# Kernel optimization log

Hardware: AMD Instinct MI355X
Metric: run time of the kernel (lower is better)

The kernel has to match this reference:

```python
import jax, jax.numpy as jnp
import numpy as np

B, L, D = 2048, 64, 300   # batch, words per sentence, embedding dim (== kernel_size)
C = 512                    # conv out_channels
H, O = 2048, 1             # fc hidden, fc output


def setup_inputs() -> dict:
    key = jax.random.key(0)
    ks = jax.random.split(key, 8)
    s = 0.05
    return {
        "x1": jax.random.normal(ks[0], (B, L, D), jnp.float32),
        "x2": jax.random.normal(ks[1], (B, L, D), jnp.float32),
        # Conv1d(in=1, out=C, kernel=D) weight is [C,1,D]; stored as [C,D]
        "Wc": jax.random.normal(ks[2], (C, D), jnp.float32) * s,
        "bc": jax.random.normal(ks[3], (C,), jnp.float32) * s,
        "W1": jax.random.normal(ks[4], (H, 2 * C), jnp.float32) * s,
        "b1": jax.random.normal(ks[5], (H,), jnp.float32) * s,
        "W2": jax.random.normal(ks[6], (O, H), jnp.float32) * s,
        "b2": jax.random.normal(ks[7], (O,), jnp.float32) * s,
    }


def reference(x1, x2, Wc, bc, W1, b1, W2, b2):
    # Per-word Conv1d(kernel=D) + ReLU is a full-width filter == linear map D->C.
    # Batch all words in one einsum instead of the original Python loop.
    def encode(x):
        h = jax.nn.relu(jnp.einsum('bld,cd->blc', x, Wc) + bc)  # [B,L,C]
        return jnp.max(h, axis=1)                                # max over words -> [B,C]

    e1 = encode(x1)
    e2 = encode(x2)
    feat = jnp.concatenate([e1 - e2, e1 * e2], axis=1)           # [B,2C]
    h = jnp.tanh(feat @ W1.T + b1)                               # [B,H]
    return h @ W2.T + b2                                         # [B,O]
```

## Files before the change

### kernel.cpp

```cpp
#include <hip/hip_runtime.h>


#define B_SZ 2048
#define L_SZ 64
#define D_SZ 300
#define C_SZ 512
#define H_SZ 2048
#define NKC 40
#define TILE_BYTES 76800
#define BUFSTRIDE 76928

typedef __bf16 bf16x8 __attribute__((ext_vector_type(8)));
typedef float f32x4 __attribute__((ext_vector_type(4)));

__device__ __forceinline__ unsigned short f2bf(float f) {
  unsigned int u = __float_as_uint(f);
  u += 0x7fffu + ((u >> 16) & 1u);
  return (unsigned short)(u >> 16);
}

__device__ __forceinline__ bf16x8 cvt8(float4 v0, float4 v1) {
  bf16x8 r;
  r[0] = (__bf16)v0.x; r[1] = (__bf16)v0.y; r[2] = (__bf16)v0.z; r[3] = (__bf16)v0.w;
  r[4] = (__bf16)v1.x; r[5] = (__bf16)v1.y; r[6] = (__bf16)v1.z; r[7] = (__bf16)v1.w;
  return r;
}

__device__ __forceinline__ void gload_lds16(const float* g, void* l) {
  __builtin_amdgcn_global_load_lds(
      (const __attribute__((address_space(1))) void*)g,
      (__attribute__((address_space(3))) void*)l, 16, 0, 0);
}

__global__ __launch_bounds__(256)
void convert_kernel(const float* __restrict__ Wc, const float* __restrict__ W1,
                    const float* __restrict__ b2,
                    unsigned short* __restrict__ WcSwz, unsigned short* __restrict__ W1Swz,
                    float* __restrict__ out) {
  int id = blockIdx.x * 256 + threadIdx.x;
  if (id < B_SZ) out[id] = b2[0];
  if (id < C_SZ * NKC) {
    int c = id / NKC, kc = id - c * NKC;
    unsigned short tmp[8];
    #pragma unroll
    for (int i = 0; i < 8; ++i) {
      int k = kc * 8 + i;
      tmp[i] = (k < D_SZ) ? f2bf(Wc[c * D_SZ + k]) : (unsigned short)0;
    }
    unsigned short* dst = WcSwz + (((c >> 4) * NKC + kc) * 16 + (c & 15)) * 8;
    *reinterpret_cast<uint4*>(dst) = *reinterpret_cast<uint4*>(tmp);
    return;
  }
  id -= C_SZ * NKC;
  if (id < H_SZ * 128) {
    int j = id >> 7, kc = id & 127;
    const float* src = W1 + (size_t)j * 1024 + kc * 8;
    unsigned short tmp[8];
    #pragma unroll
    for (int i = 0; i < 8; ++i) tmp[i] = f2bf(src[i]);
    unsigned short* dst = W1Swz + (((j >> 4) * 128 + kc) * 16 + (j & 15)) * 8;
    *reinterpret_cast<uint4*>(dst) = *reinterpret_cast<uint4*>(tmp);
  }
}

__global__ __launch_bounds__(512, 2)
void encode_feat_kernel(const float* __restrict__ x1, const float* __restrict__ x2,
                        const unsigned short* __restrict__ WcSwz,
                        const float* __restrict__ bc,
                        unsigned short* __restrict__ featSwz) {
  __shared__ __align__(16) char lds_pool[2 * BUFSTRIDE + 4096];
  float* fs = reinterpret_cast<float*>(lds_pool + 2 * BUFSTRIDE);
  const int tid = threadIdx.x;
  const int wave = tid >> 6, lane = tid & 63;
  const int l16 = lane & 15, quad = lane >> 4;

  if (tid < 16) {
    int bbuf = tid >> 3, o = (tid & 7) * 16;
    *reinterpret_cast<uint4*>(lds_pool + bbuf * BUFSTRIDE + TILE_BYTES + o) =
        make_uint4(0, 0, 0, 0);
  }

  bf16x8 breg[4][10];
  #pragma unroll
  for (int nt = 0; nt < 4; ++nt)
    #pragma unroll
    for (int ks = 0; ks < 10; ++ks)
      breg[nt][ks] = *reinterpret_cast<const bf16x8*>(
          WcSwz + (size_t)(wave * 4 + nt) * 5120 + (ks * 4 + quad) * 128 + l16 * 8);

  float bias[4];
  #pragma unroll
  for (int nt = 0; nt < 4; ++nt) bias[nt] = bc[wave * 64 + nt * 16 + l16];

  {
    const float* xb = x1 + (size_t)blockIdx.x * (L_SZ * D_SZ);
    for (int j = wave; j < 75; j += 8)
      gload_lds16(xb + j * 256 + lane * 4, lds_pool + j * 1024);
  }
  asm volatile("s_waitcnt vmcnt(0)" ::: "memory");
  __syncthreads();

  float e1[4];
  int buf = 0;

  for (int t = 0; t < 16; ++t) {
    if (t < 15) {
      int tn = t + 1;
      const float* xb = ((tn & 1) ? x2 : x1) +
                        (size_t)(blockIdx.x + (tn >> 1) * 256) * (L_SZ * D_SZ);
      char* dst = lds_pool + (buf ^ 1) * BUFSTRIDE;
      for (int j = wave; j < 75; j += 8)
        gload_lds16(xb + j * 256 + lane * 4, dst + j * 1024);
    }

    const char* xt = lds_pool + buf * BUFSTRIDE;
    float erun[4] = {0.f, 0.f, 0.f, 0.f};
    #pragma unroll
    for (int mt = 0; mt < 4; ++mt) {
      f32x4 acc[4];
      #pragma unroll
      for (int nt = 0; nt < 4; ++nt)
        #pragma unroll
        for (int r = 0; r < 4; ++r) acc[nt][r] = 0.f;
      #pragma unroll
      for (int ks = 0; ks < 10; ++ks) {
        const char* p = xt + (mt * 16 + l16) * 1200 + ks * 128 + quad * 32;
        float4 v0 = *reinterpret_cast<const float4*>(p);
        float4 v1 = *reinterpret_cast<const float4*>(p + 16);
        bf16x8 a = cvt8(v0, v1);
        #pragma unroll
        for (int nt = 0; nt < 4; ++nt)
          acc[nt] = __builtin_amdgcn_mfma_f32_16x16x32_bf16(a, breg[nt][ks], acc[nt], 0, 0, 0);
      }
      #pragma unroll
      for (int nt = 0; nt < 4; ++nt)
        #pragma unroll
        for (int r = 0; r < 4; ++r)
          erun[nt] = fmaxf(erun[nt], acc[nt][r] + bias[nt]);
    }

    #pragma unroll
    for (int nt = 0; nt < 4; ++nt) {
      float v = erun[nt];
      v = fmaxf(v, __shfl_xor(v, 16));
      v = fmaxf(v, __shfl_xor(v, 32));
      if (!(t & 1)) {
        e1[nt] = v;
      } else if (quad == 0) {
        int c = wave * 64 + nt * 16 + l16;
        fs[c]       = e1[nt] - v;
        fs[512 + c] = e1[nt] * v;
      }
    }

    __syncthreads();

    if ((t & 1) && tid < 128) {
      int b = blockIdx.x + (t >> 1) * 256;
      unsigned short tmp[8];
      #pragma unroll
      for (int i = 0; i < 8; ++i) tmp[i] = f2bf(fs[tid * 8 + i]);
      *reinterpret_cast<uint4*>(featSwz + (((b >> 4) * 128 + tid) * 16 + (b & 15)) * 8) =
          *reinterpret_cast<uint4*>(tmp);
    }
    buf ^= 1;
  }
}

__global__ __launch_bounds__(256, 4)
void fc1_kernel(const unsigned short* __restrict__ featSwz,
                const unsigned short* __restrict__ W1Swz,
                const float* __restrict__ b1, const float* __restrict__ W2,
                float* __restrict__ out) {
  const int mbase = blockIdx.x * 32;
  const int tid = threadIdx.x;
  const int wave = tid >> 6, lane = tid & 63;
  const int l16 = lane & 15, quad = lane >> 4;
  const int nbase = blockIdx.y * 128 + wave * 32;

  f32x4 acc[2][2];
  #pragma unroll
  for (int mt = 0; mt < 2; ++mt)
    #pragma unroll
    for (int nt = 0; nt < 2; ++nt)
      #pragma unroll
      for (int r = 0; r < 4; ++r) acc[mt][nt][r] = 0.f;

  #pragma unroll 4
  for (int ks = 0; ks < 32; ++ks) {
    bf16x8 a[2], bw[2];
    #pragma unroll
    for (int mt = 0; mt < 2; ++mt)
      a[mt] = *reinterpret_cast<const bf16x8*>(
          featSwz + (((size_t)(blockIdx.x * 2 + mt) * 128 + ks * 4 + quad) * 16 + l16) * 8);
    #pragma unroll
    for (int nt = 0; nt < 2; ++nt)
      bw[nt] = *reinterpret_cast<const bf16x8*>(
          W1Swz + (((size_t)(blockIdx.y * 8 + wave * 2 + nt) * 128 + ks * 4 + quad) * 16 + l16) * 8);
    #pragma unroll
    for (int mt = 0; mt < 2; ++mt)
      #pragma unroll
      for (int nt = 0; nt < 2; ++nt)
        acc[mt][nt] = __builtin_amdgcn_mfma_f32_16x16x32_bf16(a[mt], bw[nt], acc[mt][nt], 0, 0, 0);
  }

  float c[2][4];
  #pragma unroll
  for (int mt = 0; mt < 2; ++mt)
    #pragma unroll
    for (int r = 0; r < 4; ++r) c[mt][r] = 0.f;

  #pragma unroll
  for (int nt = 0; nt < 2; ++nt) {
    int j = nbase + nt * 16 + l16;
    float bias = b1[j];
    float w2 = W2[j];
    #pragma unroll
    for (int mt = 0; mt < 2; ++mt)
      #pragma unroll
      for (int r = 0; r < 4; ++r) {
        float pre = acc[mt][nt][r] + bias;
        pre = fminf(fmaxf(pre, -15.f), 15.f);
        float ex = __expf(2.f * pre);
        c[mt][r] += w2 * ((ex - 1.f) / (ex + 1.f));
      }
  }
  #pragma unroll
  for (int off = 1; off <= 8; off <<= 1)
    #pragma unroll
    for (int mt = 0; mt < 2; ++mt)
      #pragma unroll
      for (int r = 0; r < 4; ++r)
        c[mt][r] += __shfl_xor(c[mt][r], off);

  if (l16 == 0) {
    #pragma unroll
    for (int mt = 0; mt < 2; ++mt)
      #pragma unroll
      for (int r = 0; r < 4; ++r) {
        int brow = mbase + mt * 16 + quad * 4 + r;
        atomicAdd(&out[brow], c[mt][r]);
      }
  }
}

extern "C" void kernel_launch(void* const* d_in, const int* in_sizes, int n_in,
                              void* d_out, int out_size, void* d_ws, size_t ws_size,
                              hipStream_t stream) {
  const float* x1 = (const float*)d_in[0];
  const float* x2 = (const float*)d_in[1];
  const float* Wc = (const float*)d_in[2];
  const float* bc = (const float*)d_in[3];
  const float* W1 = (const float*)d_in[4];
  const float* b1 = (const float*)d_in[5];
  const float* W2 = (const float*)d_in[6];
  const float* b2 = (const float*)d_in[7];

  char* ws = (char*)d_ws;
  unsigned short* WcSwz   = (unsigned short*)(ws);
  unsigned short* W1Swz   = (unsigned short*)(ws + 327680);
  unsigned short* featSwz = (unsigned short*)(ws + 4521984);

  {
    int total = C_SZ * NKC + H_SZ * 128;
    convert_kernel<<<(total + 255) / 256, 256, 0, stream>>>(Wc, W1, b2, WcSwz, W1Swz,
                                                            (float*)d_out);
  }
  encode_feat_kernel<<<256, 512, 0, stream>>>(x1, x2, WcSwz, bc, featSwz);
  fc1_kernel<<<dim3(B_SZ / 32, H_SZ / 128), 256, 0, stream>>>(featSwz, W1Swz, b1, W2,
                                                              (float*)d_out);
}
```

Baseline: 455.6 us.

## Stage input tiles as pre-converted swizzled bf16 via register prefetch

Replaces the direct global-to-LDS fp32 copies with register prefetch of the next tile, split into two halves. Each half is converted to bf16 and written into an MFMA-swizzled LDS layout between compute phases. This halves LDS footprint and read traffic and removes per-use conversion in the inner loop, since each element is converted once instead of once per wave. The cost is extra register pressure for the prefetch buffers, scattered 8-byte LDS stores, and the loss of the asynchronous LDS-direct load path.

```diff
diff --git a/kernel.cpp b/kernel.cpp
--- a/kernel.cpp
+++ b/kernel.cpp
@@ -7,29 +7,15 @@
 #define C_SZ 512
 #define H_SZ 2048
 #define NKC 40
-#define TILE_BYTES 76800
-#define BUFSTRIDE 76928
 
 typedef __bf16 bf16x8 __attribute__((ext_vector_type(8)));
+typedef __bf16 bf16x4 __attribute__((ext_vector_type(4)));
 typedef float f32x4 __attribute__((ext_vector_type(4)));
 
 __device__ __forceinline__ unsigned short f2bf(float f) {
   unsigned int u = __float_as_uint(f);
   u += 0x7fffu + ((u >> 16) & 1u);
   return (unsigned short)(u >> 16);
-}
-
-__device__ __forceinline__ bf16x8 cvt8(float4 v0, float4 v1) {
-  bf16x8 r;
-  r[0] = (__bf16)v0.x; r[1] = (__bf16)v0.y; r[2] = (__bf16)v0.z; r[3] = (__bf16)v0.w;
-  r[4] = (__bf16)v1.x; r[5] = (__bf16)v1.y; r[6] = (__bf16)v1.z; r[7] = (__bf16)v1.w;
-  return r;
-}
-
-__device__ __forceinline__ void gload_lds16(const float* g, void* l) {
-  __builtin_amdgcn_global_load_lds(
-      (const __attribute__((address_space(1))) void*)g,
-      (__attribute__((address_space(3))) void*)l, 16, 0, 0);
 }
 
 __global__ __launch_bounds__(256)
@@ -68,16 +54,19 @@
                         const unsigned short* __restrict__ WcSwz,
                         const float* __restrict__ bc,
                         unsigned short* __restrict__ featSwz) {
-  __shared__ __align__(16) char lds_pool[2 * BUFSTRIDE + 4096];
-  float* fs = reinterpret_cast<float*>(lds_pool + 2 * BUFSTRIDE);
+  __shared__ __align__(16) unsigned short xs[2][4 * NKC * 16 * 8];
+  __shared__ float fs[1024];
   const int tid = threadIdx.x;
   const int wave = tid >> 6, lane = tid & 63;
   const int l16 = lane & 15, quad = lane >> 4;
 
-  if (tid < 16) {
-    int bbuf = tid >> 3, o = (tid & 7) * 16;
-    *reinterpret_cast<uint4*>(lds_pool + bbuf * BUFSTRIDE + TILE_BYTES + o) =
-        make_uint4(0, 0, 0, 0);
+  if (tid < 384) {
+    int bbuf = tid / 192, j = tid % 192;
+    int s = j % 3, rem = j / 3, mt = rem >> 4, l = rem & 15;
+    int kc = 37 + s;
+    unsigned short* p = &xs[bbuf][((mt * NKC + kc) * 16 + l) * 8];
+    if (s == 0) *reinterpret_cast<uint2*>(p + 4) = make_uint2(0, 0);
+    else        *reinterpret_cast<uint4*>(p)     = make_uint4(0, 0, 0, 0);
   }
 
   bf16x8 breg[4][10];
@@ -92,31 +81,46 @@
   #pragma unroll
   for (int nt = 0; nt < 4; ++nt) bias[nt] = bc[wave * 64 + nt * 16 + l16];
 
-  {
-    const float* xb = x1 + (size_t)blockIdx.x * (L_SZ * D_SZ);
-    for (int j = wave; j < 75; j += 8)
-      gload_lds16(xb + j * 256 + lane * 4, lds_pool + j * 1024);
-  }
-  asm volatile("s_waitcnt vmcnt(0)" ::: "memory");
+  float4 pf[5];
+  auto LOADG = [&](int t, int r0) {
+    const float* xb = ((t & 1) ? x2 : x1) +
+                      (size_t)(blockIdx.x + (t >> 1) * 256) * (L_SZ * D_SZ);
+    #pragma unroll
+    for (int r = 0; r < 5; ++r) {
+      int idx = (r0 + r) * 512 + tid;
+      if (idx < 4800) pf[r] = *reinterpret_cast<const float4*>(xb + idx * 4);
+    }
+  };
+  auto WRITEG = [&](int bbuf, int r0) {
+    #pragma unroll
+    for (int r = 0; r < 5; ++r) {
+      int idx = (r0 + r) * 512 + tid;
+      if (idx < 4800) {
+        int row = idx / 75, c4 = idx - row * 75;
+        int mt = row >> 4, l = row & 15, kc = c4 >> 1;
+        bf16x4 c;
+        c[0] = (__bf16)pf[r].x; c[1] = (__bf16)pf[r].y;
+        c[2] = (__bf16)pf[r].z; c[3] = (__bf16)pf[r].w;
+        *reinterpret_cast<bf16x4*>(
+            &xs[bbuf][((mt * NKC + kc) * 16 + l) * 8 + (c4 & 1) * 4]) = c;
+      }
+    }
+  };
+
+  LOADG(0, 0); WRITEG(0, 0);
+  LOADG(0, 5); WRITEG(0, 5);
   __syncthreads();
 
   float e1[4];
   int buf = 0;
 
   for (int t = 0; t < 16; ++t) {
-    if (t < 15) {
-      int tn = t + 1;
-      const float* xb = ((tn & 1) ? x2 : x1) +
-                        (size_t)(blockIdx.x + (tn >> 1) * 256) * (L_SZ * D_SZ);
-      char* dst = lds_pool + (buf ^ 1) * BUFSTRIDE;
-      for (int j = wave; j < 75; j += 8)
-        gload_lds16(xb + j * 256 + lane * 4, dst + j * 1024);
-    }
-
-    const char* xt = lds_pool + buf * BUFSTRIDE;
+    if (t < 15) LOADG(t + 1, 0);
+
     float erun[4] = {0.f, 0.f, 0.f, 0.f};
-    #pragma unroll
-    for (int mt = 0; mt < 4; ++mt) {
+
+    #pragma unroll
+    for (int mt = 0; mt < 2; ++mt) {
       f32x4 acc[4];
       #pragma unroll
       for (int nt = 0; nt < 4; ++nt)
@@ -124,10 +128,8 @@
         for (int r = 0; r < 4; ++r) acc[nt][r] = 0.f;
       #pragma unroll
       for (int ks = 0; ks < 10; ++ks) {
-        const char* p = xt + (mt * 16 + l16) * 1200 + ks * 128 + quad * 32;
-        float4 v0 = *reinterpret_cast<const float4*>(p);
-        float4 v1 = *reinterpret_cast<const float4*>(p + 16);
-        bf16x8 a = cvt8(v0, v1);
+        bf16x8 a = *reinterpret_cast<const bf16x8*>(
+            &xs[buf][mt * 5120 + (ks * 4 + quad) * 128 + l16 * 8]);
         #pragma unroll
         for (int nt = 0; nt < 4; ++nt)
           acc[nt] = __builtin_amdgcn_mfma_f32_16x16x32_bf16(a, breg[nt][ks], acc[nt], 0, 0, 0);
@@ -138,6 +140,32 @@
         for (int r = 0; r < 4; ++r)
           erun[nt] = fmaxf(erun[nt], acc[nt][r] + bias[nt]);
     }
+
+    if (t < 15) { WRITEG(buf ^ 1, 0); LOADG(t + 1, 5); }
+
+    #pragma unroll
+    for (int mt = 2; mt < 4; ++mt) {
+      f32x4 acc[4];
+      #pragma unroll
+      for (int nt = 0; nt < 4; ++nt)
+        #pragma unroll
+        for (int r = 0; r < 4; ++r) acc[nt][r] = 0.f;
+      #pragma unroll
+      for (int ks = 0; ks < 10; ++ks) {
+        bf16x8 a = *reinterpret_cast<const bf16x8*>(
+            &xs[buf][mt * 5120 + (ks * 4 + quad) * 128 + l16 * 8]);
+        #pragma unroll
+        for (int nt = 0; nt < 4; ++nt)
+          acc[nt] = __builtin_amdgcn_mfma_f32_16x16x32_bf16(a, breg[nt][ks], acc[nt], 0, 0, 0);
+      }
+      #pragma unroll
+      for (int nt = 0; nt < 4; ++nt)
+        #pragma unroll
+        for (int r = 0; r < 4; ++r)
+          erun[nt] = fmaxf(erun[nt], acc[nt][r] + bias[nt]);
+    }
+
+    if (t < 15) WRITEG(buf ^ 1, 5);
 
     #pragma unroll
     for (int nt = 0; nt < 4; ++nt) {
```

Measured after the change: 562.6 us. 23.5% more time.
